# Kernel tuning notes

Hardware: AMD Instinct MI355X
Metric: run time of the kernel (lower is better)

Reference implementation:

```python
import jax, jax.numpy as jnp
import numpy as np

CHANNELS = 1024
T_LEN = 16384
WINDOW = 16
W_MIN, W_MAX = -1.0, 3.0
BETA = 0.95       # snn.Leaky(beta=0.95)
THRESHOLD = 1.0   # snn.Leaky(threshold=1)


def setup_inputs() -> dict:
    key = jax.random.key(0)
    inp = jax.random.normal(key, (CHANNELS, T_LEN), dtype=jnp.float32)
    return {"inp": inp}


def reference(inp):
    C, T = inp.shape
    pad = WINDOW // 2
    inp_padded = jnp.pad(inp, ((0, 0), (pad, pad)))  # [C, T + WINDOW]
    n_steps = T - WINDOW

    def step(carry, t):
        w, mem = carry
        # B: sliding window [C, WINDOW] starting at column t of padded input
        B = jax.lax.dynamic_slice(inp_padded, (0, t), (C, WINDOW))
        # mean(B @ B.T, axis=1) == B @ mean(B, axis=0)  -- avoids [C, C] intermediate
        B_ram = B @ jnp.mean(B, axis=0)
        w = jnp.clip(0.5 * w + 0.5 * B_ram, W_MIN, W_MAX)
        x = B[:, 0]  # == inp_padded[:, t]
        # snntorch Leaky, reset_mechanism='subtract':
        # reset from incoming mem, then mem = beta*mem + input - reset*thr, spk = mem > thr
        reset = (mem > THRESHOLD).astype(inp.dtype)
        mem = BETA * mem + w * x - reset * THRESHOLD
        spk = (mem > THRESHOLD).astype(inp.dtype)
        return (w, mem), spk

    w0 = jnp.ones((C,), dtype=inp.dtype)
    mem0 = jnp.zeros((C,), dtype=inp.dtype)
    _, spks = jax.lax.scan(step, (w0, mem0), jnp.arange(n_steps))  # spks: [n_steps, C]
    # out = deepcopy(inp); out[:, t] = spk for t < T - WINDOW
    out = inp.at[:, :n_steps].set(spks.T)
    return out
```

## Files before the change

kernel.cpp:

```cpp
#include <hip/hip_runtime.h>
#include <stdint.h>

#define C_CH   1024
#define T_DIM  16384
#define NSTEPS (T_DIM - 16)
#define PAD    8
#define TP     (T_DIM + 16)
#define SEG    256

#define WS_CM_OFFSET (8u * T_DIM * sizeof(double))

__global__ __launch_bounds__(128) void colsum_partial(const float* __restrict__ inp,
                                                      double* __restrict__ part) {
    int col4 = (blockIdx.x * 128 + threadIdx.x) * 4;
    int rc   = blockIdx.y;
    const float* p = inp + (size_t)rc * 128 * T_DIM + col4;
    double ax = 0.0, ay = 0.0, az = 0.0, aw = 0.0;
    #pragma unroll 16
    for (int r = 0; r < 128; ++r) {
        float4 v = *(const float4*)(p + (size_t)r * T_DIM);
        ax += (double)v.x; ay += (double)v.y; az += (double)v.z; aw += (double)v.w;
    }
    double* q = part + (size_t)rc * T_DIM + col4;
    q[0] = ax; q[1] = ay; q[2] = az; q[3] = aw;
}

__global__ void colmean_tail(const double* __restrict__ part, const float* __restrict__ inp,
                             float* __restrict__ cm, float* __restrict__ out) {
    int i = blockIdx.x * 256 + threadIdx.x;
    if (i < TP) {
        float v = 0.0f;
        if (i >= PAD && i < T_DIM + PAD) {
            int col = i - PAD;
            double t = 0.0;
            #pragma unroll
            for (int r = 0; r < 8; ++r) t += part[(size_t)r * T_DIM + col];
            v = (float)(t * (1.0 / 1024.0));
        }
        cm[i] = v;
    }
    if (i < C_CH * 16) {
        int c = i >> 4, j = i & 15;
        size_t idx = (size_t)c * T_DIM + NSTEPS + j;
        out[idx] = inp[idx];
    }
}

__device__ __forceinline__ float4 swz_ld(const float* base, int b) {
    int a = (b & ~1023) | ((((b >> 4) & 63) ^ ((b >> 10) & 7)) << 4);
    return *(const float4*)((const char*)base + a);
}

__global__ __launch_bounds__(64) void scan_kernel(const float* __restrict__ inp,
                                                  const float* __restrict__ cm,
                                                  float* __restrict__ out) {
    __shared__ float    rowl[T_DIM + 8];
    __shared__ uint32_t bm[64][8];

    const int ch   = blockIdx.x;
    const int lane = threadIdx.x;
    const float* row  = inp + (size_t)ch * T_DIM;
    float*       orow = out + (size_t)ch * T_DIM;

    #pragma unroll
    for (int i = 0; i < 64; ++i) {
        const float* src = row + i * SEG + ((lane ^ (i & 7)) << 2);
        __builtin_amdgcn_global_load_lds(
            (const __attribute__((address_space(1))) void*)src,
            (__attribute__((address_space(3))) void*)(rowl + i * SEG),
            16, 0, 0);
    }
    if (lane < 2) {
        *(float4*)(rowl + T_DIM + lane * 4) = make_float4(0.f, 0.f, 0.f, 0.f);
    }
    asm volatile("s_waitcnt vmcnt(0)" ::: "memory");
    __builtin_amdgcn_sched_barrier(0);

    const int sW = (lane == 0) ? 0 : (lane - 1) * SEG;
    const int sM = lane * SEG;

    float xs[16], ms[16];
    {
        const float4* cp = (const float4*)(cm + sW);
        float4 m0 = cp[0], m1 = cp[1], m2 = cp[2], m3 = cp[3];
        float mt[16] = {m0.x,m0.y,m0.z,m0.w, m1.x,m1.y,m1.z,m1.w,
                        m2.x,m2.y,m2.z,m2.w, m3.x,m3.y,m3.z,m3.w};
        #pragma unroll
        for (int j = 0; j < 16; ++j) ms[j] = mt[j];

        if (sW == 0) {
            float4 x2 = swz_ld(rowl, 0);
            float4 x3 = swz_ld(rowl, 16);
            float xt[8] = {x2.x,x2.y,x2.z,x2.w, x3.x,x3.y,x3.z,x3.w};
            #pragma unroll
            for (int j = 0; j < 8; ++j) { xs[j] = 0.0f; xs[j + 8] = xt[j]; }
        } else {
            const int b = sW * 4 - 32;
            float4 x0 = swz_ld(rowl, b),      x1 = swz_ld(rowl, b + 16),
                   x2 = swz_ld(rowl, b + 32), x3 = swz_ld(rowl, b + 48);
            float xt[16] = {x0.x,x0.y,x0.z,x0.w, x1.x,x1.y,x1.z,x1.w,
                            x2.x,x2.y,x2.z,x2.w, x3.x,x3.y,x3.z,x3.w};
            #pragma unroll
            for (int j = 0; j < 16; ++j) xs[j] = xt[j];
        }
    }
    float win = 0.0f;
    #pragma unroll
    for (int j = 0; j < 16; ++j) win = fmaf(xs[j], ms[j], win);

    float w = 1.0f, mem = 0.0f, spf = 0.0f;

    for (int it = 0; it < 16; ++it) {
        if (lane != 0) {
            const int b = sW * 4 + it * 64 + 32;
            float4 a0 = swz_ld(rowl, b),      a1 = swz_ld(rowl, b + 16),
                   a2 = swz_ld(rowl, b + 32), a3 = swz_ld(rowl, b + 48);
            const float4* cp = (const float4*)(cm + sW + it * 16 + 16);
            float4 b0 = cp[0], b1 = cp[1], b2 = cp[2], b3 = cp[3];
            float xn[16] = {a0.x,a0.y,a0.z,a0.w, a1.x,a1.y,a1.z,a1.w,
                            a2.x,a2.y,a2.z,a2.w, a3.x,a3.y,a3.z,a3.w};
            float mn[16] = {b0.x,b0.y,b0.z,b0.w, b1.x,b1.y,b1.z,b1.w,
                            b2.x,b2.y,b2.z,b2.w, b3.x,b3.y,b3.z,b3.w};
            #pragma unroll
            for (int j = 0; j < 16; ++j) {
                w = fminf(fmaxf(fmaf(0.5f, w, 0.5f * win), -1.0f), 3.0f);
                float x = xs[j];
                mem = fmaf(0.95f, mem, fmaf(w, x, -spf));
                spf = (mem > 1.0f) ? 1.0f : 0.0f;
                win = fmaf(xn[j], mn[j], fmaf(-x, ms[j], win));
                xs[j] = xn[j]; ms[j] = mn[j];
            }
        }
    }

    uint32_t sb[8] = {0, 0, 0, 0, 0, 0, 0, 0};
    #pragma unroll
    for (int q = 0; q < 16; ++q) {
        const int b = sM * 4 + q * 64 + 32;
        float4 a0 = swz_ld(rowl, b),      a1 = swz_ld(rowl, b + 16),
               a2 = swz_ld(rowl, b + 32), a3 = swz_ld(rowl, b + 48);
        const float4* cp = (const float4*)(cm + sM + q * 16 + 16);
        float4 b0 = cp[0], b1 = cp[1], b2 = cp[2], b3 = cp[3];
        float xn[16] = {a0.x,a0.y,a0.z,a0.w, a1.x,a1.y,a1.z,a1.w,
                        a2.x,a2.y,a2.z,a2.w, a3.x,a3.y,a3.z,a3.w};
        float mn[16] = {b0.x,b0.y,b0.z,b0.w, b1.x,b1.y,b1.z,b1.w,
                        b2.x,b2.y,b2.z,b2.w, b3.x,b3.y,b3.z,b3.w};
        uint32_t m16 = 0;
        #pragma unroll
        for (int j = 0; j < 16; ++j) {
            w = fminf(fmaxf(fmaf(0.5f, w, 0.5f * win), -1.0f), 3.0f);
            float x = xs[j];
            mem = fmaf(0.95f, mem, fmaf(w, x, -spf));
            bool sp = (mem > 1.0f);
            spf = sp ? 1.0f : 0.0f;
            m16 |= sp ? (1u << j) : 0u;
            win = fmaf(xn[j], mn[j], fmaf(-x, ms[j], win));
            xs[j] = xn[j]; ms[j] = mn[j];
        }
        sb[q >> 1] |= m16 << ((q & 1) * 16);
    }

    *(uint4*)&bm[lane][0] = make_uint4(sb[0], sb[1], sb[2], sb[3]);
    *(uint4*)&bm[lane][4] = make_uint4(sb[4], sb[5], sb[6], sb[7]);
    #pragma unroll 8
    for (int seg = 0; seg < 64; ++seg) {
        uint32_t word = bm[seg][lane >> 3];
        uint32_t bits = (word >> ((lane & 7) * 4)) & 0xFu;
        float4 v = make_float4((bits & 1u) ? 1.f : 0.f, (bits & 2u) ? 1.f : 0.f,
                               (bits & 4u) ? 1.f : 0.f, (bits & 8u) ? 1.f : 0.f);
        if (seg < 63 || lane < 60)
            *(float4*)(orow + seg * SEG + lane * 4) = v;
    }
}

extern "C" void kernel_launch(void* const* d_in, const int* in_sizes, int n_in,
                              void* d_out, int out_size, void* d_ws, size_t ws_size,
                              hipStream_t stream) {
    const float* inp = (const float*)d_in[0];
    float* out = (float*)d_out;
    double* part = (double*)d_ws;
    float* cm = (float*)((char*)d_ws + WS_CM_OFFSET);

    colsum_partial<<<dim3(32, 8), 128, 0, stream>>>(inp, part);
    colmean_tail<<<dim3(65), 256, 0, stream>>>(part, inp, cm, out);
    scan_kernel<<<dim3(C_CH), 64, 0, stream>>>(inp, cm, out);
}
```

Baseline: 157.0 us.

## Split each channel scan across 256 threads with short segments, drop LDS staging

Each channel's time scan now runs on 256 threads, each owning a 64-step segment, where before 64 threads each owned 256 steps. Every thread warms up over at most 256 preceding steps to converge the clipped weight state. The whole-row LDS staging through global_load_lds is removed, so inputs are read straight from global memory and cache. The aim is a shorter serial chain per thread and more wavefronts per CU. The cost is redundant warm-up work, more global loads, and reliance on w converging within the warm-up window.

```diff
diff --git a/kernel.cpp b/kernel.cpp
--- a/kernel.cpp
+++ b/kernel.cpp
@@ -6,7 +6,7 @@
 #define NSTEPS (T_DIM - 16)
 #define PAD    8
 #define TP     (T_DIM + 16)
-#define SEG    256
+#define SEG    64
 
 #define WS_CM_OFFSET (8u * T_DIM * sizeof(double))
 
@@ -46,58 +46,39 @@
     }
 }
 
-__device__ __forceinline__ float4 swz_ld(const float* base, int b) {
-    int a = (b & ~1023) | ((((b >> 4) & 63) ^ ((b >> 10) & 7)) << 4);
-    return *(const float4*)((const char*)base + a);
-}
+__global__ __launch_bounds__(256, 4) void scan_kernel(const float* __restrict__ inp,
+                                                      const float* __restrict__ cm,
+                                                      float* __restrict__ out) {
+    __shared__ uint32_t bm[256][2];
 
-__global__ __launch_bounds__(64) void scan_kernel(const float* __restrict__ inp,
-                                                  const float* __restrict__ cm,
-                                                  float* __restrict__ out) {
-    __shared__ float    rowl[T_DIM + 8];
-    __shared__ uint32_t bm[64][8];
-
-    const int ch   = blockIdx.x;
-    const int lane = threadIdx.x;
+    const int ch = blockIdx.x;
+    const int l  = threadIdx.x;
     const float* row  = inp + (size_t)ch * T_DIM;
     float*       orow = out + (size_t)ch * T_DIM;
 
-    #pragma unroll
-    for (int i = 0; i < 64; ++i) {
-        const float* src = row + i * SEG + ((lane ^ (i & 7)) << 2);
-        __builtin_amdgcn_global_load_lds(
-            (const __attribute__((address_space(1))) void*)src,
-            (__attribute__((address_space(3))) void*)(rowl + i * SEG),
-            16, 0, 0);
-    }
-    if (lane < 2) {
-        *(float4*)(rowl + T_DIM + lane * 4) = make_float4(0.f, 0.f, 0.f, 0.f);
-    }
-    asm volatile("s_waitcnt vmcnt(0)" ::: "memory");
-    __builtin_amdgcn_sched_barrier(0);
-
-    const int sW = (lane == 0) ? 0 : (lane - 1) * SEG;
-    const int sM = lane * SEG;
+    const int t0  = l << 6;
+    const int nwu = min(16, t0 >> 4);
+    const int tw  = t0 - (nwu << 4);
 
     float xs[16], ms[16];
     {
-        const float4* cp = (const float4*)(cm + sW);
+        const float4* cp = (const float4*)(cm + tw);
         float4 m0 = cp[0], m1 = cp[1], m2 = cp[2], m3 = cp[3];
         float mt[16] = {m0.x,m0.y,m0.z,m0.w, m1.x,m1.y,m1.z,m1.w,
                         m2.x,m2.y,m2.z,m2.w, m3.x,m3.y,m3.z,m3.w};
         #pragma unroll
         for (int j = 0; j < 16; ++j) ms[j] = mt[j];
 
-        if (sW == 0) {
-            float4 x2 = swz_ld(rowl, 0);
-            float4 x3 = swz_ld(rowl, 16);
+        if (tw == 0) {
+            float4 x2 = *(const float4*)(row);
+            float4 x3 = *(const float4*)(row + 4);
             float xt[8] = {x2.x,x2.y,x2.z,x2.w, x3.x,x3.y,x3.z,x3.w};
             #pragma unroll
             for (int j = 0; j < 8; ++j) { xs[j] = 0.0f; xs[j + 8] = xt[j]; }
         } else {
-            const int b = sW * 4 - 32;
-            float4 x0 = swz_ld(rowl, b),      x1 = swz_ld(rowl, b + 16),
-                   x2 = swz_ld(rowl, b + 32), x3 = swz_ld(rowl, b + 48);
+            const float* rp = row + tw - 8;
+            float4 x0 = *(const float4*)(rp),     x1 = *(const float4*)(rp + 4),
+                   x2 = *(const float4*)(rp + 8), x3 = *(const float4*)(rp + 12);
             float xt[16] = {x0.x,x0.y,x0.z,x0.w, x1.x,x1.y,x1.z,x1.w,
                             x2.x,x2.y,x2.z,x2.w, x3.x,x3.y,x3.z,x3.w};
             #pragma unroll
@@ -110,36 +91,45 @@
 
     float w = 1.0f, mem = 0.0f, spf = 0.0f;
 
-    for (int it = 0; it < 16; ++it) {
-        if (lane != 0) {
-            const int b = sW * 4 + it * 64 + 32;
-            float4 a0 = swz_ld(rowl, b),      a1 = swz_ld(rowl, b + 16),
-                   a2 = swz_ld(rowl, b + 32), a3 = swz_ld(rowl, b + 48);
-            const float4* cp = (const float4*)(cm + sW + it * 16 + 16);
-            float4 b0 = cp[0], b1 = cp[1], b2 = cp[2], b3 = cp[3];
-            float xn[16] = {a0.x,a0.y,a0.z,a0.w, a1.x,a1.y,a1.z,a1.w,
-                            a2.x,a2.y,a2.z,a2.w, a3.x,a3.y,a3.z,a3.w};
-            float mn[16] = {b0.x,b0.y,b0.z,b0.w, b1.x,b1.y,b1.z,b1.w,
-                            b2.x,b2.y,b2.z,b2.w, b3.x,b3.y,b3.z,b3.w};
-            #pragma unroll
-            for (int j = 0; j < 16; ++j) {
-                w = fminf(fmaxf(fmaf(0.5f, w, 0.5f * win), -1.0f), 3.0f);
-                float x = xs[j];
-                mem = fmaf(0.95f, mem, fmaf(w, x, -spf));
-                spf = (mem > 1.0f) ? 1.0f : 0.0f;
-                win = fmaf(xn[j], mn[j], fmaf(-x, ms[j], win));
-                xs[j] = xn[j]; ms[j] = mn[j];
-            }
+    for (int it = 0; it < nwu; ++it) {
+        const int t = tw + (it << 4);
+        const float* rp = row + t + 8;
+        float4 a0 = *(const float4*)(rp),      a1 = *(const float4*)(rp + 4),
+               a2 = *(const float4*)(rp + 8),  a3 = *(const float4*)(rp + 12);
+        const float4* cp = (const float4*)(cm + t + 16);
+        float4 b0 = cp[0], b1 = cp[1], b2 = cp[2], b3 = cp[3];
+        float xn[16] = {a0.x,a0.y,a0.z,a0.w, a1.x,a1.y,a1.z,a1.w,
+                        a2.x,a2.y,a2.z,a2.w, a3.x,a3.y,a3.z,a3.w};
+        float mn[16] = {b0.x,b0.y,b0.z,b0.w, b1.x,b1.y,b1.z,b1.w,
+                        b2.x,b2.y,b2.z,b2.w, b3.x,b3.y,b3.z,b3.w};
+        #pragma unroll
+        for (int j = 0; j < 16; ++j) {
+            w = fminf(fmaxf(fmaf(0.5f, w, 0.5f * win), -1.0f), 3.0f);
+            float x = xs[j];
+            mem = fmaf(0.95f, mem, fmaf(w, x, -spf));
+            spf = (mem > 1.0f) ? 1.0f : 0.0f;
+            win = fmaf(xn[j], mn[j], fmaf(-x, ms[j], win));
+            xs[j] = xn[j]; ms[j] = mn[j];
         }
     }
 
-    uint32_t sb[8] = {0, 0, 0, 0, 0, 0, 0, 0};
+    uint32_t sb0 = 0, sb1 = 0;
     #pragma unroll
-    for (int q = 0; q < 16; ++q) {
-        const int b = sM * 4 + q * 64 + 32;
-        float4 a0 = swz_ld(rowl, b),      a1 = swz_ld(rowl, b + 16),
-               a2 = swz_ld(rowl, b + 32), a3 = swz_ld(rowl, b + 48);
-        const float4* cp = (const float4*)(cm + sM + q * 16 + 16);
+    for (int q = 0; q < 4; ++q) {
+        const int t = t0 + (q << 4);
+        const float* rp = row + t + 8;
+        float4 a0 = *(const float4*)(rp), a1 = *(const float4*)(rp + 4);
+        float4 a2, a3;
+        if (q == 3) {
+            const int p2 = t + 16, p3 = t + 20;
+            a2 = *(const float4*)(row + min(p2, T_DIM - 4));
+            a3 = *(const float4*)(row + min(p3, T_DIM - 4));
+            if (p2 >= T_DIM) a2 = make_float4(0.f, 0.f, 0.f, 0.f);
+            if (p3 >= T_DIM) a3 = make_float4(0.f, 0.f, 0.f, 0.f);
+        } else {
+            a2 = *(const float4*)(rp + 8); a3 = *(const float4*)(rp + 12);
+        }
+        const float4* cp = (const float4*)(cm + t + 16);
         float4 b0 = cp[0], b1 = cp[1], b2 = cp[2], b3 = cp[3];
         float xn[16] = {a0.x,a0.y,a0.z,a0.w, a1.x,a1.y,a1.z,a1.w,
                         a2.x,a2.y,a2.z,a2.w, a3.x,a3.y,a3.z,a3.w};
@@ -157,19 +147,23 @@
             win = fmaf(xn[j], mn[j], fmaf(-x, ms[j], win));
             xs[j] = xn[j]; ms[j] = mn[j];
         }
-        sb[q >> 1] |= m16 << ((q & 1) * 16);
+        if (q < 2) sb0 |= m16 << (q * 16);
+        else       sb1 |= m16 << ((q - 2) * 16);
     }
 
-    *(uint4*)&bm[lane][0] = make_uint4(sb[0], sb[1], sb[2], sb[3]);
-    *(uint4*)&bm[lane][4] = make_uint4(sb[4], sb[5], sb[6], sb[7]);
-    #pragma unroll 8
-    for (int seg = 0; seg < 64; ++seg) {
-        uint32_t word = bm[seg][lane >> 3];
-        uint32_t bits = (word >> ((lane & 7) * 4)) & 0xFu;
-        float4 v = make_float4((bits & 1u) ? 1.f : 0.f, (bits & 2u) ? 1.f : 0.f,
-                               (bits & 4u) ? 1.f : 0.f, (bits & 8u) ? 1.f : 0.f);
-        if (seg < 63 || lane < 60)
-            *(float4*)(orow + seg * SEG + lane * 4) = v;
+    bm[l][0] = sb0; bm[l][1] = sb1;
+    __syncthreads();
+    #pragma unroll
+    for (int k = 0; k < 16; ++k) {
+        const int p = k * 1024 + (l << 2);
+        uint32_t word = bm[p >> 6][(p >> 5) & 1];
+        uint32_t bits = (word >> (p & 31)) & 0xFu;
+        if (k < 15 || l < 252) {
+            *(float4*)(orow + p) = make_float4((bits & 1u) ? 1.f : 0.f,
+                                               (bits & 2u) ? 1.f : 0.f,
+                                               (bits & 4u) ? 1.f : 0.f,
+                                               (bits & 8u) ? 1.f : 0.f);
+        }
     }
 }
 
@@ -183,5 +177,5 @@
 
     colsum_partial<<<dim3(32, 8), 128, 0, stream>>>(inp, part);
     colmean_tail<<<dim3(65), 256, 0, stream>>>(part, inp, cm, out);
-    scan_kernel<<<dim3(C_CH), 64, 0, stream>>>(inp, cm, out);
+    scan_kernel<<<dim3(C_CH), 256, 0, stream>>>(inp, cm, out);
 }
```

Result: slower. 244.7 us (+55.9%).

## Restructure column-mean reduction into more partial groups and move tail copy into scan

Applied to the files above, without the earlier changes.

The column-sum stage now splits rows into 64 groups of 16 with 256-thread blocks over 4096-column chunks, raising parallelism from 256 small blocks to 256 larger blocks with more independent loads each. A second kernel reduces the 64 partials per column with coalesced reads. The partial buffer is placed in the output buffer (overwritten later by the scan), and the copy of the final 16 columns moves into the scan kernel. This aims to cut the latency of the serial pre-pass ahead of the scan, at the cost of more partial-sum traffic and reliance on the output buffer as scratch.

```diff
diff --git a/kernel.cpp b/kernel.cpp
--- a/kernel.cpp
+++ b/kernel.cpp
@@ -4,46 +4,47 @@
 #define C_CH   1024
 #define T_DIM  16384
 #define NSTEPS (T_DIM - 16)
-#define PAD    8
 #define TP     (T_DIM + 16)
 #define SEG    256
 
-#define WS_CM_OFFSET (8u * T_DIM * sizeof(double))
 
-__global__ __launch_bounds__(128) void colsum_partial(const float* __restrict__ inp,
+__global__ __launch_bounds__(256) void colsum_partial(const float* __restrict__ inp,
                                                       double* __restrict__ part) {
-    int col4 = (blockIdx.x * 128 + threadIdx.x) * 4;
-    int rc   = blockIdx.y;
-    const float* p = inp + (size_t)rc * 128 * T_DIM + col4;
-    double ax = 0.0, ay = 0.0, az = 0.0, aw = 0.0;
-    #pragma unroll 16
-    for (int r = 0; r < 128; ++r) {
-        float4 v = *(const float4*)(p + (size_t)r * T_DIM);
-        ax += (double)v.x; ay += (double)v.y; az += (double)v.z; aw += (double)v.w;
+    const int q = blockIdx.x, g = blockIdx.y, t = threadIdx.x;
+    const int c0 = q * 4096;
+    const float* p = inp + (size_t)(g * 16) * T_DIM + c0;
+    double acc[4][4];
+    #pragma unroll
+    for (int i = 0; i < 4; ++i)
+        #pragma unroll
+        for (int j = 0; j < 4; ++j) acc[i][j] = 0.0;
+    #pragma unroll 4
+    for (int r = 0; r < 16; ++r) {
+        const float* pr = p + (size_t)r * T_DIM;
+        #pragma unroll
+        for (int i = 0; i < 4; ++i) {
+            float4 v = *(const float4*)(pr + (i * 256 + t) * 4);
+            acc[i][0] += v.x; acc[i][1] += v.y; acc[i][2] += v.z; acc[i][3] += v.w;
+        }
     }
-    double* q = part + (size_t)rc * T_DIM + col4;
-    q[0] = ax; q[1] = ay; q[2] = az; q[3] = aw;
+    double* qp = part + (size_t)g * T_DIM + c0;
+    #pragma unroll
+    for (int i = 0; i < 4; ++i) {
+        *(double2*)(qp + (i * 256 + t) * 4)     = make_double2(acc[i][0], acc[i][1]);
+        *(double2*)(qp + (i * 256 + t) * 4 + 2) = make_double2(acc[i][2], acc[i][3]);
+    }
 }
 
-__global__ void colmean_tail(const double* __restrict__ part, const float* __restrict__ inp,
-                             float* __restrict__ cm, float* __restrict__ out) {
-    int i = blockIdx.x * 256 + threadIdx.x;
-    if (i < TP) {
-        float v = 0.0f;
-        if (i >= PAD && i < T_DIM + PAD) {
-            int col = i - PAD;
-            double t = 0.0;
-            #pragma unroll
-            for (int r = 0; r < 8; ++r) t += part[(size_t)r * T_DIM + col];
-            v = (float)(t * (1.0 / 1024.0));
-        }
-        cm[i] = v;
-    }
-    if (i < C_CH * 16) {
-        int c = i >> 4, j = i & 15;
-        size_t idx = (size_t)c * T_DIM + NSTEPS + j;
-        out[idx] = inp[idx];
-    }
+__global__ __launch_bounds__(256) void colmean_coal(const double* __restrict__ part,
+                                                    float* __restrict__ cm) {
+    const int b = blockIdx.x, t = threadIdx.x;
+    const int col = b * 256 + t;
+    double s = 0.0;
+    #pragma unroll 8
+    for (int r = 0; r < 64; ++r) s += part[(size_t)r * T_DIM + col];
+    cm[8 + col] = (float)(s * (1.0 / 1024.0));
+    if (b == 0 && t < 8) cm[t] = 0.0f;
+    if (b == 1 && t < 8) cm[T_DIM + 8 + t] = 0.0f;
 }
 
 __device__ __forceinline__ float4 swz_ld(const float* base, int b) {
@@ -171,6 +172,7 @@
         if (seg < 63 || lane < 60)
             *(float4*)(orow + seg * SEG + lane * 4) = v;
     }
+    if (lane < 16) orow[NSTEPS + lane] = row[NSTEPS + lane];
 }
 
 extern "C" void kernel_launch(void* const* d_in, const int* in_sizes, int n_in,
@@ -178,10 +180,10 @@
                               hipStream_t stream) {
     const float* inp = (const float*)d_in[0];
     float* out = (float*)d_out;
-    double* part = (double*)d_ws;
-    float* cm = (float*)((char*)d_ws + WS_CM_OFFSET);
+    double* part = (double*)d_out;
+    float* cm  = (float*)d_ws;
 
-    colsum_partial<<<dim3(32, 8), 128, 0, stream>>>(inp, part);
-    colmean_tail<<<dim3(65), 256, 0, stream>>>(part, inp, cm, out);
+    colsum_partial<<<dim3(4, 64), 256, 0, stream>>>(inp, part);
+    colmean_coal<<<dim3(64), 256, 0, stream>>>(part, cm);
     scan_kernel<<<dim3(C_CH), 64, 0, stream>>>(inp, cm, out);
 }
```

New measurement: 159.5 us. Within noise of the previous version (+1.6%).
